# Performance work log

Hardware: AMD Instinct MI355X
Metric: run time of the kernel (lower is better)

## Reference

```python
import jax, jax.numpy as jnp
import numpy as np

D = 1024
H = 16
DH = D // H

def setup_inputs() -> dict:
    key = jax.random.key(0)
    k1, k2, k3, k4 = jax.random.split(key, 4)
    x = jax.random.normal(k1, (4, 2048, D), dtype=jnp.float32)
    # qkv_linear: Linear(D, D, bias=False); weight stored as (out, in) torch-style
    w_qkv = jax.random.normal(k2, (D, D), dtype=jnp.float32) * (1.0 / np.sqrt(D))
    # final linear: Linear(D, D) with bias
    w_out = jax.random.normal(k3, (D, D), dtype=jnp.float32) * (1.0 / np.sqrt(D))
    b_out = jax.random.normal(k4, (D,), dtype=jnp.float32) * 0.01
    return {"x": x, "w_qkv": w_qkv, "w_out": w_out, "b_out": b_out}

def reference(x, w_qkv, w_out, b_out):
    B, S, E = x.shape
    # Same projection used for Q, K, V (faithful to original module)
    qkv = jnp.einsum('bse,de->bsd', x, w_qkv)           # [B,S,D]
    qkv = qkv.reshape(B, S, H, DH).transpose(0, 2, 1, 3)  # [B,H,S,Dh]
    q = k = v = qkv
    scale = DH ** -0.5
    attn = jnp.einsum('bhqd,bhkd->bhqk', q, k) * scale   # [B,H,S,S]
    attn = jax.nn.softmax(attn, axis=-1)
    out = jnp.einsum('bhqk,bhkd->bhqd', attn, v)         # [B,H,S,Dh]
    out = out.transpose(0, 2, 1, 3).reshape(B, S, E)
    return jnp.einsum('bse,de->bsd', out, w_out) + b_out
```

## Files before the change

kernel.cpp:

```cpp
#include <hip/hip_runtime.h>
#include <hip/hip_bf16.h>
#include <stdint.h>

typedef unsigned short u16;
typedef unsigned int   u32;
typedef unsigned long long u64;
typedef __bf16 bf16x8 __attribute__((ext_vector_type(8)));
typedef float  f32x4  __attribute__((ext_vector_type(4)));
typedef short  s16x4  __attribute__((ext_vector_type(4)));

#define D_MODEL 1024
#define NH 16
#define DHEAD 64
#define BB 4
#define SS 2048
#define MM (BB*SS)

__device__ __forceinline__ u16 f2bf(float f) {
    unsigned int u = __float_as_uint(f);
    u += 0x7fffu + ((u >> 16) & 1u);
    return (u16)(u >> 16);
}
__device__ __forceinline__ float bf2f(u16 s) {
    return __uint_as_float(((unsigned int)s) << 16);
}
__device__ __forceinline__ u32 pkbf(float a, float b) {
    __hip_bfloat162 h = __float22bfloat162_rn(make_float2(a, b));
    return *(u32*)&h;
}

union U8 {
    uint4 q;
    u16   v[8];
    bf16x8 f;
};
union B8 { u32 w[4]; bf16x8 f; };
union V8 { s16x4 h[2]; bf16x8 f; };

#define N4X (MM * D_MODEL / 4)
#define N4W (D_MODEL * D_MODEL / 4)
__global__ __launch_bounds__(256) void cvt_all_kernel(const float* __restrict__ x,
                                                      const float* __restrict__ wq,
                                                      const float* __restrict__ wo,
                                                      u16* __restrict__ xb,
                                                      u16* __restrict__ wqb,
                                                      u16* __restrict__ wob) {
    int i = blockIdx.x * 256 + threadIdx.x;
    const float* s; u16* d; int off;
    if (i < N4X)            { s = x;  d = xb;  off = i; }
    else if (i < N4X + N4W) { s = wq; d = wqb; off = i - N4X; }
    else                    { s = wo; d = wob; off = i - N4X - N4W; }
    float4 f = ((const float4*)s)[off];
    u32 o[2] = { pkbf(f.x, f.y), pkbf(f.z, f.w) };
    ((uint2*)d)[off] = *(const uint2*)o;
}

template <bool PERMUTE_OUT>
__device__ __forceinline__ void gemm_body(const u16* __restrict__ A,
                                          const u16* __restrict__ Bt,
                                          const float* __restrict__ Bo,
                                          u16* __restrict__ Cq, u16* __restrict__ CqT,
                                          float* __restrict__ Out)
{
    __shared__ __align__(16) u16 As[128*64];
    __shared__ __align__(16) u16 Bs[128*64];

    const int tid  = threadIdx.x;
    const int wave = tid >> 6;
    const int lane = tid & 63;
    const int quad = lane >> 4;
    const int l16  = lane & 15;
    const int dsw = blockIdx.x;
    const int sl  = dsw >> 3;
    const int bm  = ((sl >> 3) << 3) + (dsw & 7);
    const int bn  = sl & 7;
    const int wm = wave >> 1, wn = wave & 1;

    f32x4 acc[4][4] = {};

    const int rp = tid >> 3;
    const int ch = tid & 7;
    const int sc = ch ^ (rp & 7);

    const u16* Ab = A  + (size_t)(bm * 128 + rp) * D_MODEL + sc * 8;
    const u16* Bb = Bt + (size_t)(bn * 128 + rp) * D_MODEL + sc * 8;
    const int xr = l16 & 7;

    for (int k0 = 0; k0 < D_MODEL; k0 += 64) {
#pragma unroll
        for (int p = 0; p < 4; ++p) {
            __builtin_amdgcn_global_load_lds(
                (__attribute__((address_space(1))) void*)(Ab + (size_t)(32*p) * D_MODEL + k0),
                (__attribute__((address_space(3))) void*)(As + p*2048 + tid*8), 16, 0, 0);
            __builtin_amdgcn_global_load_lds(
                (__attribute__((address_space(1))) void*)(Bb + (size_t)(32*p) * D_MODEL + k0),
                (__attribute__((address_space(3))) void*)(Bs + p*2048 + tid*8), 16, 0, 0);
        }
        __syncthreads();

#pragma unroll
        for (int ks = 0; ks < 2; ++ks) {
            bf16x8 af[4], bfr[4];
#pragma unroll
            for (int t = 0; t < 4; ++t)
                af[t] = *(const bf16x8*)(const void*)(
                    As + (wm*64 + t*16 + l16)*64 + (((ks*4 + quad) ^ xr) * 8));
#pragma unroll
            for (int t = 0; t < 4; ++t)
                bfr[t] = *(const bf16x8*)(const void*)(
                    Bs + (wn*64 + t*16 + l16)*64 + (((ks*4 + quad) ^ xr) * 8));
#pragma unroll
            for (int i = 0; i < 4; ++i)
#pragma unroll
                for (int j = 0; j < 4; ++j)
                    acc[i][j] = __builtin_amdgcn_mfma_f32_16x16x32_bf16(af[i], bfr[j], acc[i][j], 0, 0, 0);
        }
        __syncthreads();
    }

    const int rowbase = bm*128 + wm*64;
    const int colbase = bn*128 + wn*64;
    if (PERMUTE_OUT) {
#pragma unroll
        for (int j = 0; j < 4; ++j) {
            const int col = colbase + j*16 + l16;
            const int h = col >> 6, dh = col & 63;
#pragma unroll
            for (int i = 0; i < 4; ++i) {
                const int row0 = rowbase + i*16 + quad*4;
                const int b = row0 >> 11, s0 = row0 & (SS - 1);
#pragma unroll
                for (int r = 0; r < 4; ++r)
                    Cq[(((size_t)(b*NH + h))*SS + s0 + r)*DHEAD + dh] = f2bf(acc[i][j][r]);
                u64 w = (u64)pkbf(acc[i][j][0], acc[i][j][1])
                      | ((u64)pkbf(acc[i][j][2], acc[i][j][3]) << 32);
                *(u64*)(CqT + ((size_t)((b*NH + h)*DHEAD + dh))*SS + s0) = w;
            }
        }
    } else {
#pragma unroll
        for (int j = 0; j < 4; ++j) {
            const int col = colbase + j*16 + l16;
            const float bias = Bo[col];
#pragma unroll
            for (int i = 0; i < 4; ++i) {
#pragma unroll
                for (int r = 0; r < 4; ++r) {
                    const int row = rowbase + i*16 + quad*4 + r;
                    Out[(size_t)row * D_MODEL + col] = acc[i][j][r] + bias;
                }
            }
        }
    }
}

__global__ __launch_bounds__(256) void gemm_qkv_kernel(const u16* __restrict__ A,
                                                       const u16* __restrict__ Bt,
                                                       u16* __restrict__ Cq,
                                                       u16* __restrict__ CqT) {
    gemm_body<true>(A, Bt, nullptr, Cq, CqT, nullptr);
}

__global__ __launch_bounds__(256) void gemm_out_kernel(const u16* __restrict__ A,
                                                       const u16* __restrict__ Bt,
                                                       const float* __restrict__ Bo,
                                                       float* __restrict__ Out) {
    gemm_body<false>(A, Bt, Bo, nullptr, nullptr, Out);
}

__global__ __launch_bounds__(256, 4) void attn_kernel(const u16* __restrict__ qkv,
                                                      const u16* __restrict__ qkvT,
                                                      u16* __restrict__ outb)
{
    __shared__ __align__(16) u16 Ks[2*2048];
    __shared__ __align__(16) u16 Vt[2*2048];

    const int tid  = threadIdx.x;
    const int wave = tid >> 6;
    const int lane = tid & 63;
    const int quad = lane >> 4;
    const int l16  = lane & 15;

    const int dsw  = blockIdx.x;
    const int sl   = dsw >> 3;
    const int bh   = ((sl >> 4) << 3) + (dsw & 7);
    const int qblk = sl & 15;
    const int b = bh >> 4, h = bh & 15;
    const int qbase = qblk * 128 + wave * 32;

    const u16* Qp = qkv + (size_t)bh * SS * DHEAD;
    const float qscale = 0.125f * 1.4426950408889634f;

    bf16x8 qb[2][2];
#pragma unroll
    for (int nt = 0; nt < 2; ++nt)
#pragma unroll
        for (int ks = 0; ks < 2; ++ks) {
            U8 raw; raw.q = *(const uint4*)(Qp + (size_t)(qbase + nt*16 + l16)*DHEAD + ks*32 + quad*8);
            U8 w;
#pragma unroll
            for (int jj = 0; jj < 4; ++jj)
                ((u32*)&w)[jj] = pkbf(bf2f(raw.v[2*jj]) * qscale, bf2f(raw.v[2*jj+1]) * qscale);
            qb[nt][ks] = w.f;
        }

    const int rK = tid >> 3, cK = (tid & 7) ^ ((rK >> 1) & 7);
    const u16* srcK = qkv  + (size_t)bh * SS * DHEAD + rK * DHEAD + cK * 8;
    const int rV = tid >> 2, cV = (tid & 3) ^ ((rV >> 1) & 3);
    const u16* srcV = qkvT + (size_t)bh * DHEAD * SS + (size_t)rV * SS + cV * 8;

    const int h8 = (l16 >> 1) & 7, h4 = (l16 >> 1) & 3;
    const int ko0 = l16*64 + ((quad)     ^ h8) * 8;
    const int ko1 = l16*64 + ((4 + quad) ^ h8) * 8;
    const int vo0 = l16*32 + (((quad >> 1))     ^ h4) * 8 + (quad & 1) * 4;
    const int vo1 = l16*32 + ((2 + (quad >> 1)) ^ h4) * 8 + (quad & 1) * 4;

    f32x4 ot[4][2] = {};
    float lacc[2]  = {0.0f, 0.0f};

    __builtin_amdgcn_global_load_lds(
        (__attribute__((address_space(1))) void*)(srcK),
        (__attribute__((address_space(3))) void*)(Ks + tid*8), 16, 0, 0);
    __builtin_amdgcn_global_load_lds(
        (__attribute__((address_space(1))) void*)(srcV),
        (__attribute__((address_space(3))) void*)(Vt + tid*8), 16, 0, 0);

#pragma unroll 2
    for (int kt = 0; kt < SS/32; ++kt) {
        __syncthreads();
        if (kt < SS/32 - 1) {
            __builtin_amdgcn_global_load_lds(
                (__attribute__((address_space(1))) void*)(srcK + (size_t)(kt+1)*32*DHEAD),
                (__attribute__((address_space(3))) void*)(Ks + ((kt+1)&1)*2048 + tid*8), 16, 0, 0);
            __builtin_amdgcn_global_load_lds(
                (__attribute__((address_space(1))) void*)(srcV + (kt+1)*32),
                (__attribute__((address_space(3))) void*)(Vt + ((kt+1)&1)*2048 + tid*8), 16, 0, 0);
        }
        const u16* Kb = Ks + (kt&1)*2048;
        const u16* Vb = Vt + (kt&1)*2048;

        V8 vt[4];
#pragma unroll
        for (int dt = 0; dt < 4; ++dt) {
            vt[dt].h[0] = *(const s16x4*)(const void*)(Vb + dt*512 + vo0);
            vt[dt].h[1] = *(const s16x4*)(const void*)(Vb + dt*512 + vo1);
        }

        f32x4 s[2][2] = {};
        __builtin_amdgcn_s_setprio(1);
#pragma unroll
        for (int mt = 0; mt < 2; ++mt) {
            bf16x8 kf0 = *(const bf16x8*)(const void*)(Kb + mt*1024 + ko0);
            bf16x8 kf1 = *(const bf16x8*)(const void*)(Kb + mt*1024 + ko1);
#pragma unroll
            for (int nt = 0; nt < 2; ++nt)
                s[mt][nt] = __builtin_amdgcn_mfma_f32_16x16x32_bf16(kf0, qb[nt][0], s[mt][nt], 0, 0, 0);
#pragma unroll
            for (int nt = 0; nt < 2; ++nt)
                s[mt][nt] = __builtin_amdgcn_mfma_f32_16x16x32_bf16(kf1, qb[nt][1], s[mt][nt], 0, 0, 0);
        }
        __builtin_amdgcn_s_setprio(0);

        bf16x8 pb[2];
#pragma unroll
        for (int nt = 0; nt < 2; ++nt) {
            float p00 = __builtin_amdgcn_exp2f(s[0][nt][0]);
            float p01 = __builtin_amdgcn_exp2f(s[0][nt][1]);
            float p02 = __builtin_amdgcn_exp2f(s[0][nt][2]);
            float p03 = __builtin_amdgcn_exp2f(s[0][nt][3]);
            float p10 = __builtin_amdgcn_exp2f(s[1][nt][0]);
            float p11 = __builtin_amdgcn_exp2f(s[1][nt][1]);
            float p12 = __builtin_amdgcn_exp2f(s[1][nt][2]);
            float p13 = __builtin_amdgcn_exp2f(s[1][nt][3]);
            lacc[nt] += ((p00 + p01) + (p02 + p03)) + ((p10 + p11) + (p12 + p13));
            B8 t;
            t.w[0] = pkbf(p00, p01); t.w[1] = pkbf(p02, p03);
            t.w[2] = pkbf(p10, p11); t.w[3] = pkbf(p12, p13);
            pb[nt] = t.f;
        }

        __builtin_amdgcn_s_setprio(1);
#pragma unroll
        for (int dt = 0; dt < 4; ++dt) {
            ot[dt][0] = __builtin_amdgcn_mfma_f32_16x16x32_bf16(vt[dt].f, pb[0], ot[dt][0], 0, 0, 0);
            ot[dt][1] = __builtin_amdgcn_mfma_f32_16x16x32_bf16(vt[dt].f, pb[1], ot[dt][1], 0, 0, 0);
        }
        __builtin_amdgcn_s_setprio(0);
    }

    float inv[2];
#pragma unroll
    for (int nt = 0; nt < 2; ++nt) {
        float v = lacc[nt];
        v += __shfl_xor(v, 16, 64);
        v += __shfl_xor(v, 32, 64);
        inv[nt] = 1.0f / v;
    }

#pragma unroll
    for (int dt = 0; dt < 4; ++dt)
#pragma unroll
        for (int nt = 0; nt < 2; ++nt) {
            u64 w = (u64)pkbf(ot[dt][nt][0]*inv[nt], ot[dt][nt][1]*inv[nt])
                  | ((u64)pkbf(ot[dt][nt][2]*inv[nt], ot[dt][nt][3]*inv[nt]) << 32);
            *(u64*)(outb + ((size_t)(b*SS + qbase + nt*16 + l16))*D_MODEL
                         + h*64 + dt*16 + quad*4) = w;
        }
}

extern "C" void kernel_launch(void* const* d_in, const int* in_sizes, int n_in,
                              void* d_out, int out_size, void* d_ws, size_t ws_size,
                              hipStream_t stream)
{
    (void)in_sizes; (void)n_in; (void)out_size; (void)ws_size;
    const float* x  = (const float*)d_in[0];
    const float* wq = (const float*)d_in[1];
    const float* wo = (const float*)d_in[2];
    const float* bo = (const float*)d_in[3];

    char* ws = (char*)d_ws;
    u16* xb    = (u16*)(ws);
    u16* wqb   = (u16*)(ws + (size_t)(16 << 20));
    u16* wob   = (u16*)(ws + (size_t)(18 << 20));
    u16* qkvb  = (u16*)(ws + (size_t)(20 << 20));
    u16* qkvTb = (u16*)(ws + (size_t)(36 << 20));
    u16* attb  = xb;

    cvt_all_kernel<<<(N4X + 2*N4W) / 256, 256, 0, stream>>>(x, wq, wo, xb, wqb, wob);
    gemm_qkv_kernel<<<(MM/128) * (D_MODEL/128), 256, 0, stream>>>(xb, wqb, qkvb, qkvTb);
    attn_kernel<<<BB * NH * (SS/128), 256, 0, stream>>>(qkvb, qkvTb, attb);
    gemm_out_kernel<<<(MM/128) * (D_MODEL/128), 256, 0, stream>>>(attb, wob, bo, (float*)d_out);
}
```

Baseline: 227.5 us.

## Double per-wave query tile in attention and compute row sums via MFMA

Each attention wave now handles 64 query rows instead of 32, so every K/V tile loaded into LDS is reused across twice as many queries and the grid is halved. Softmax denominators are accumulated with an extra MFMA against a vector of ones, which replaces the scalar adds and cross-lane shuffles. Register pressure roughly doubles (the launch bound drops to 2 blocks per SIMD set), which lowers occupancy and latency hiding. Summing the bf16-rounded probabilities also changes the normalisation slightly.

```diff
diff --git a/kernel.cpp b/kernel.cpp
--- a/kernel.cpp
+++ b/kernel.cpp
@@ -168,7 +168,7 @@
     gemm_body<false>(A, Bt, Bo, nullptr, nullptr, Out);
 }
 
-__global__ __launch_bounds__(256, 4) void attn_kernel(const u16* __restrict__ qkv,
+__global__ __launch_bounds__(256, 2) void attn_kernel(const u16* __restrict__ qkv,
                                                       const u16* __restrict__ qkvT,
                                                       u16* __restrict__ outb)
 {
@@ -183,17 +183,17 @@
 
     const int dsw  = blockIdx.x;
     const int sl   = dsw >> 3;
-    const int bh   = ((sl >> 4) << 3) + (dsw & 7);
-    const int qblk = sl & 15;
+    const int bh   = ((sl >> 3) << 3) + (dsw & 7);
+    const int qblk = sl & 7;
     const int b = bh >> 4, h = bh & 15;
-    const int qbase = qblk * 128 + wave * 32;
+    const int qbase = qblk * 256 + wave * 64;
 
     const u16* Qp = qkv + (size_t)bh * SS * DHEAD;
     const float qscale = 0.125f * 1.4426950408889634f;
 
-    bf16x8 qb[2][2];
-#pragma unroll
-    for (int nt = 0; nt < 2; ++nt)
+    bf16x8 qb[4][2];
+#pragma unroll
+    for (int nt = 0; nt < 4; ++nt)
 #pragma unroll
         for (int ks = 0; ks < 2; ++ks) {
             U8 raw; raw.q = *(const uint4*)(Qp + (size_t)(qbase + nt*16 + l16)*DHEAD + ks*32 + quad*8);
@@ -215,8 +215,12 @@
     const int vo0 = l16*32 + (((quad >> 1))     ^ h4) * 8 + (quad & 1) * 4;
     const int vo1 = l16*32 + ((2 + (quad >> 1)) ^ h4) * 8 + (quad & 1) * 4;
 
-    f32x4 ot[4][2] = {};
-    float lacc[2]  = {0.0f, 0.0f};
+    bf16x8 ones;
+#pragma unroll
+    for (int j = 0; j < 8; ++j) ones[j] = (__bf16)1.0f;
+
+    f32x4 ot[4][4] = {};
+    f32x4 lsum[4]  = {};
 
     __builtin_amdgcn_global_load_lds(
         (__attribute__((address_space(1))) void*)(srcK),
@@ -246,61 +250,50 @@
             vt[dt].h[1] = *(const s16x4*)(const void*)(Vb + dt*512 + vo1);
         }
 
-        f32x4 s[2][2] = {};
-        __builtin_amdgcn_s_setprio(1);
+        B8 pb[4];
 #pragma unroll
         for (int mt = 0; mt < 2; ++mt) {
             bf16x8 kf0 = *(const bf16x8*)(const void*)(Kb + mt*1024 + ko0);
             bf16x8 kf1 = *(const bf16x8*)(const void*)(Kb + mt*1024 + ko1);
-#pragma unroll
-            for (int nt = 0; nt < 2; ++nt)
-                s[mt][nt] = __builtin_amdgcn_mfma_f32_16x16x32_bf16(kf0, qb[nt][0], s[mt][nt], 0, 0, 0);
-#pragma unroll
-            for (int nt = 0; nt < 2; ++nt)
-                s[mt][nt] = __builtin_amdgcn_mfma_f32_16x16x32_bf16(kf1, qb[nt][1], s[mt][nt], 0, 0, 0);
-        }
-        __builtin_amdgcn_s_setprio(0);
-
-        bf16x8 pb[2];
-#pragma unroll
-        for (int nt = 0; nt < 2; ++nt) {
-            float p00 = __builtin_amdgcn_exp2f(s[0][nt][0]);
-            float p01 = __builtin_amdgcn_exp2f(s[0][nt][1]);
-            float p02 = __builtin_amdgcn_exp2f(s[0][nt][2]);
-            float p03 = __builtin_amdgcn_exp2f(s[0][nt][3]);
-            float p10 = __builtin_amdgcn_exp2f(s[1][nt][0]);
-            float p11 = __builtin_amdgcn_exp2f(s[1][nt][1]);
-            float p12 = __builtin_amdgcn_exp2f(s[1][nt][2]);
-            float p13 = __builtin_amdgcn_exp2f(s[1][nt][3]);
-            lacc[nt] += ((p00 + p01) + (p02 + p03)) + ((p10 + p11) + (p12 + p13));
-            B8 t;
-            t.w[0] = pkbf(p00, p01); t.w[1] = pkbf(p02, p03);
-            t.w[2] = pkbf(p10, p11); t.w[3] = pkbf(p12, p13);
-            pb[nt] = t.f;
+            f32x4 s[4] = {};
+            __builtin_amdgcn_s_setprio(1);
+#pragma unroll
+            for (int nt = 0; nt < 4; ++nt)
+                s[nt] = __builtin_amdgcn_mfma_f32_16x16x32_bf16(kf0, qb[nt][0], s[nt], 0, 0, 0);
+#pragma unroll
+            for (int nt = 0; nt < 4; ++nt)
+                s[nt] = __builtin_amdgcn_mfma_f32_16x16x32_bf16(kf1, qb[nt][1], s[nt], 0, 0, 0);
+            __builtin_amdgcn_s_setprio(0);
+#pragma unroll
+            for (int nt = 0; nt < 4; ++nt) {
+                float p0 = __builtin_amdgcn_exp2f(s[nt][0]);
+                float p1 = __builtin_amdgcn_exp2f(s[nt][1]);
+                float p2 = __builtin_amdgcn_exp2f(s[nt][2]);
+                float p3 = __builtin_amdgcn_exp2f(s[nt][3]);
+                pb[nt].w[2*mt]   = pkbf(p0, p1);
+                pb[nt].w[2*mt+1] = pkbf(p2, p3);
+            }
         }
 
         __builtin_amdgcn_s_setprio(1);
 #pragma unroll
-        for (int dt = 0; dt < 4; ++dt) {
-            ot[dt][0] = __builtin_amdgcn_mfma_f32_16x16x32_bf16(vt[dt].f, pb[0], ot[dt][0], 0, 0, 0);
-            ot[dt][1] = __builtin_amdgcn_mfma_f32_16x16x32_bf16(vt[dt].f, pb[1], ot[dt][1], 0, 0, 0);
-        }
+        for (int nt = 0; nt < 4; ++nt)
+            lsum[nt] = __builtin_amdgcn_mfma_f32_16x16x32_bf16(ones, pb[nt].f, lsum[nt], 0, 0, 0);
+#pragma unroll
+        for (int dt = 0; dt < 4; ++dt)
+#pragma unroll
+            for (int nt = 0; nt < 4; ++nt)
+                ot[dt][nt] = __builtin_amdgcn_mfma_f32_16x16x32_bf16(vt[dt].f, pb[nt].f, ot[dt][nt], 0, 0, 0);
         __builtin_amdgcn_s_setprio(0);
     }
 
-    float inv[2];
-#pragma unroll
-    for (int nt = 0; nt < 2; ++nt) {
-        float v = lacc[nt];
-        v += __shfl_xor(v, 16, 64);
-        v += __shfl_xor(v, 32, 64);
-        inv[nt] = 1.0f / v;
-    }
-
+    float inv[4];
+#pragma unroll
+    for (int nt = 0; nt < 4; ++nt) inv[nt] = 1.0f / lsum[nt][0];
 #pragma unroll
     for (int dt = 0; dt < 4; ++dt)
 #pragma unroll
-        for (int nt = 0; nt < 2; ++nt) {
+        for (int nt = 0; nt < 4; ++nt) {
             u64 w = (u64)pkbf(ot[dt][nt][0]*inv[nt], ot[dt][nt][1]*inv[nt])
                   | ((u64)pkbf(ot[dt][nt][2]*inv[nt], ot[dt][nt][3]*inv[nt]) << 32);
             *(u64*)(outb + ((size_t)(b*SS + qbase + nt*16 + l16))*D_MODEL
@@ -328,6 +321,6 @@
 
     cvt_all_kernel<<<(N4X + 2*N4W) / 256, 256, 0, stream>>>(x, wq, wo, xb, wqb, wob);
     gemm_qkv_kernel<<<(MM/128) * (D_MODEL/128), 256, 0, stream>>>(xb, wqb, qkvb, qkvTb);
-    attn_kernel<<<BB * NH * (SS/128), 256, 0, stream>>>(qkvb, qkvTb, attb);
+    attn_kernel<<<BB * NH * (SS/256), 256, 0, stream>>>(qkvb, qkvTb, attb);
     gemm_out_kernel<<<(MM/128) * (D_MODEL/128), 256, 0, stream>>>(attb, wob, bo, (float*)d_out);
 }
```

Result: faster. 218.9 us (-3.8%).
